# Optimization experiments

Measured on AMD Instinct MI355X. Metric: run time of the kernel, lower is better.

Reference implementation:

```python
import jax, jax.numpy as jnp
import numpy as np

NUM_CLASSES = 3
EPS = 1e-6
POS_IOU = 0.5   # assumed thresholds of utils.match_anchors_to_targets
NEG_IOU = 0.4
NEG_RATIO = 3


def _make_anchors(H, W, stride):
    sizes = np.array([3.0, 4.0, 5.0]) * stride  # 3 anchors per location
    ys = (np.arange(H) + 0.5) * stride
    xs = (np.arange(W) + 0.5) * stride
    cy, cx = np.meshgrid(ys, xs, indexing='ij')
    cx = cx[:, :, None]
    cy = cy[:, :, None]
    s = sizes[None, None, :]
    boxes = np.stack([cx - s / 2, cy - s / 2, cx + s / 2, cy + s / 2], axis=-1)  # [H,W,A,4]
    return boxes.reshape(-1, 4).astype(np.float32)


def setup_inputs() -> dict:
    key = jax.random.key(0)
    B, G, A, C = 64, 32, 3, NUM_CLASSES
    scales = [(128, 128, 8), (64, 64, 16), (32, 32, 32)]
    ks = jax.random.split(key, 6)
    inp = {}
    for i, (H, W, s) in enumerate(scales):
        inp[f'pred{i}'] = jax.random.normal(ks[i], (B, A * (5 + C), H, W), jnp.float32)
        inp[f'anchors{i}'] = jnp.asarray(_make_anchors(H, W, s))
    c = jax.random.uniform(ks[3], (B, G, 2), minval=100.0, maxval=900.0)
    wh = jax.random.uniform(ks[4], (B, G, 2), minval=16.0, maxval=200.0)
    inp['gt_boxes'] = jnp.concatenate([c - wh / 2, c + wh / 2], axis=-1)
    inp['gt_labels'] = jax.random.randint(ks[5], (B, G), 0, C)
    return inp


def _smooth_l1(x):
    ax = jnp.abs(x)
    return jnp.where(ax < 1.0, 0.5 * x * x, ax - 0.5)


def _bce_logits(x, t):
    return jnp.maximum(x, 0.0) - x * t + jnp.log1p(jnp.exp(-jnp.abs(x)))


def _pairwise_iou(a, b):  # a [N,4], b [G,4] -> [N,G]
    lt = jnp.maximum(a[:, None, :2], b[None, :, :2])
    rb = jnp.minimum(a[:, None, 2:], b[None, :, 2:])
    wh = jnp.clip(rb - lt, 0.0)
    inter = wh[..., 0] * wh[..., 1]
    area_a = (a[:, 2] - a[:, 0]) * (a[:, 3] - a[:, 1])
    area_b = (b[:, 2] - b[:, 0]) * (b[:, 3] - b[:, 1])
    return inter / (area_a[:, None] + area_b[None, :] - inter + 1e-9)


def _per_image(p, anc, gtb, gtl):
    # p: [N, 5+C], anc: [N,4], gtb: [G,4], gtl: [G]
    iou = _pairwise_iou(anc, gtb)
    best_iou = jnp.max(iou, axis=1)
    best_idx = jnp.argmax(iou, axis=1)
    m_boxes = gtb[best_idx]
    m_labels = gtl[best_idx]
    pos = best_iou >= POS_IOU
    neg = best_iou < NEG_IOU
    posf = pos.astype(p.dtype)

    ax = (anc[:, 0] + anc[:, 2]) * 0.5
    ay = (anc[:, 1] + anc[:, 3]) * 0.5
    aw = jnp.maximum(anc[:, 2] - anc[:, 0], EPS)
    ah = jnp.maximum(anc[:, 3] - anc[:, 1], EPS)
    gx = (m_boxes[:, 0] + m_boxes[:, 2]) * 0.5
    gy = (m_boxes[:, 1] + m_boxes[:, 3]) * 0.5
    gw = jnp.maximum(m_boxes[:, 2] - m_boxes[:, 0], EPS)
    gh = jnp.maximum(m_boxes[:, 3] - m_boxes[:, 1], EPS)
    t_tx = (gx - ax) / aw
    t_ty = (gy - ay) / ah
    t_tw = jnp.log(gw / aw)
    t_th = jnp.log(gh / ah)

    loc = (posf * (_smooth_l1(p[:, 0] - t_tx) + _smooth_l1(p[:, 1] - t_ty)
                   + _smooth_l1(p[:, 2] - t_tw) + _smooth_l1(p[:, 3] - t_th))).sum()

    obj_all = _bce_logits(p[:, 4], posf)
    # hard negative mining on detached loss: top (3*max(1,num_pos)) negatives
    num_pos = pos.sum()
    num_keep = NEG_RATIO * jnp.maximum(1, num_pos)
    neg_loss = jnp.where(neg, jax.lax.stop_gradient(obj_all), -1e9)
    order = jnp.argsort(-neg_loss)
    N = order.shape[0]
    ranks = jnp.zeros((N,), dtype=jnp.int32).at[order].set(jnp.arange(N, dtype=jnp.int32))
    selected = neg & (ranks < num_keep)
    obj = (obj_all * (posf + selected.astype(p.dtype))).sum()

    logp = jax.nn.log_softmax(p[:, 5:], axis=-1)
    tgt = jnp.maximum(m_labels, 0)
    ce = -jnp.take_along_axis(logp, tgt[:, None], axis=1)[:, 0]
    cls = (posf * ce).sum()
    return loc, obj, cls


def reference(pred0, pred1, pred2, anchors0, anchors1, anchors2, gt_boxes, gt_labels):
    B = pred0.shape[0]
    C = NUM_CLASSES
    total = jnp.float32(0.0)
    for pred, anc in ((pred0, anchors0), (pred1, anchors1), (pred2, anchors2)):
        N = anc.shape[0]
        p = pred.transpose(0, 2, 3, 1).reshape(B, N, 5 + C)  # [B, H*W*A, 5+C]
        loc, obj, cls = jax.vmap(lambda pb, gb, gl, a=anc: _per_image(pb, a, gb, gl))(
            p, gt_boxes, gt_labels)
        total = total + loc.sum() + obj.sum() + cls.sum()
    return total / jnp.maximum(1.0, float(B))
```

## Files before the change

### kernel.cpp

```cpp
#include <hip/hip_runtime.h>
#include <math.h>

#define BLK 256
#define SBLK 1024
#define NBINS 2048
#define HREP 2
#define CSH 42
#define QMASK ((1ULL << CSH) - 1ULL)

__device__ __forceinline__ float bce_logits(float x, float t){
    return fmaxf(x, 0.f) - x * t + log1pf(expf(-fabsf(x)));
}
__device__ __forceinline__ float smooth_l1(float x){
    float ax = fabsf(x);
    return ax < 1.f ? 0.5f * x * x : ax - 0.5f;
}

__global__ __launch_bounds__(BLK)
void det_map_all(const float* __restrict__ pred0,
                 const float* __restrict__ pred1,
                 const float* __restrict__ pred2,
                 const float* __restrict__ gtb,
                 const int*   __restrict__ gtl,
                 unsigned long long* __restrict__ hist,
                 float* __restrict__ loss_slot,
                 int*   __restrict__ pcnt_slot,
                 unsigned* __restrict__ done_cnt,
                 int B)
{
    const int b  = blockIdx.y;
    const int bx = blockIdx.x;

    const float* pred; int s, qloc, P, logW; float stride_f;
    if (bx < 48){      s=0; pred=pred0; P=16384; logW=7; stride_f= 8.f; qloc= bx      << 8; }
    else if (bx < 60){ s=1; pred=pred1; P= 4096; logW=6; stride_f=16.f; qloc=(bx-48) << 8; }
    else {             s=2; pred=pred2; P= 1024; logW=5; stride_f=32.f; qloc=(bx-60) << 8; }

    const int tid = threadIdx.x;
    const int lq  = 2*logW - 2;
    const int Q4  = 1 << lq;
    const int a   = qloc >> lq;
    const int pix0 = (qloc - a*Q4 + tid) << 2;

    const float half = 0.5f * (float)(3 + a) * stride_f;

    const int pixLo = (qloc - a*Q4) << 2;
    const int y0 = pixLo >> logW, y1 = (pixLo + BLK*4 - 1) >> logW;
    const float ymin = ((float)y0 + 0.5f) * stride_f - half;
    const float ymax = ((float)y1 + 0.5f) * stride_f + half;

    __shared__ float4 sg[32];
    __shared__ float  sarea[32];
    __shared__ int    sl[32];
    __shared__ int    s_cnt;
    __shared__ unsigned long long sh_h[HREP][NBINS];

    for (int i = tid; i < HREP * NBINS; i += BLK)
        ((unsigned long long*)sh_h)[i] = 0ULL;

    {
        bool keep = false; float4 G;
        if (tid < 32){
            G = ((const float4*)gtb)[b * 32 + tid];
            keep = (G.y < ymax) && (G.w > ymin);
        }
        unsigned long long m = __ballot(keep);
        if (tid < 64){
            if (keep){
                int idx = (int)__popcll(m & ((1ULL << tid) - 1ULL));
                sg[idx] = G;
                sarea[idx] = (G.z - G.x) * (G.w - G.y);
                sl[idx] = gtl[b * 32 + tid];
            }
            if (tid == 0) s_cnt = (int)__popcll(m);
        }
    }
    __syncthreads();
    const int cnt = s_cnt;

    const int x0 = pix0 & ((1 << logW) - 1);
    const int y  = pix0 >> logW;
    const float cy = ((float)y + 0.5f) * stride_f;
    const float Ay = cy - half, Ay2 = cy + half;
    const float area_a = (2.f * half) * (2.f * half);

    float ax[4], az[4];
    #pragma unroll
    for (int j = 0; j < 4; ++j){
        float cx = ((float)(x0 + j) + 0.5f) * stride_f;
        ax[j] = cx - half; az[j] = cx + half;
    }

    float bi[4] = {-1.f, -1.f, -1.f, -1.f};
    float bd[4] = { 1.f,  1.f,  1.f,  1.f};
    int   bg[4] = {0, 0, 0, 0};

    for (int g = 0; g < cnt; ++g){
        const float4 G = sg[g];
        const float sab = area_a + sarea[g];
        const float h = fmaxf(fminf(Ay2, G.w) - fmaxf(Ay, G.y), 0.f);
        #pragma unroll
        for (int j = 0; j < 4; ++j){
            float wdt = fmaxf(fminf(az[j], G.z) - fmaxf(ax[j], G.x), 0.f);
            float inter = wdt * h;
            float d = (sab - inter) + 1e-9f;
            if (inter * bd[j] > bi[j] * d){ bi[j] = inter; bd[j] = d; bg[j] = g; }
        }
    }

    const size_t cP = (size_t)P;
    const float* pp = pred + ((size_t)b * 24 + (size_t)a * 8) * cP + (size_t)pix0;
    const float4 p4v = *(const float4*)(pp + 4 * cP);
    const float p4a[4] = {p4v.x, p4v.y, p4v.z, p4v.w};

    const int rep = tid & (HREP - 1);
    float loss = 0.f; int pc = 0;
    #pragma unroll
    for (int j = 0; j < 4; ++j){
        const bool pos = 2.f * bi[j] >= bd[j];
        const bool neg = bi[j] < 0.4f * bd[j];
        if (neg){
            float v = bce_logits(p4a[j], 0.f);
            int bin = min((int)(v * 512.f), NBINS - 1);
            unsigned long long pq = (1ULL << CSH) |
                (unsigned long long)(unsigned)(int)(v * 4194304.f);
            atomicAdd(&sh_h[rep][bin], pq);
        }
        if (pos){
            pc++;
            const float4 G = sg[bg[j]];
            float axc = (ax[j] + az[j]) * 0.5f, ayc = (Ay + Ay2) * 0.5f;
            float aw = fmaxf(az[j] - ax[j], 1e-6f), ah = fmaxf(Ay2 - Ay, 1e-6f);
            float gxc = (G.x + G.z) * 0.5f, gyc = (G.y + G.w) * 0.5f;
            float gw = fmaxf(G.z - G.x, 1e-6f), gh = fmaxf(G.w - G.y, 1e-6f);
            float p0 = pp[0 * cP + j];
            float p1 = pp[1 * cP + j];
            float p2 = pp[2 * cP + j];
            float p3 = pp[3 * cP + j];
            loss += smooth_l1(p0 - (gxc - axc) / aw);
            loss += smooth_l1(p1 - (gyc - ayc) / ah);
            loss += smooth_l1(p2 - logf(gw / aw));
            loss += smooth_l1(p3 - logf(gh / ah));
            loss += bce_logits(p4a[j], 1.f);
            float c0 = pp[5 * cP + j];
            float c1 = pp[6 * cP + j];
            float c2 = pp[7 * cP + j];
            float m = fmaxf(c0, fmaxf(c1, c2));
            float lse = m + logf(expf(c0 - m) + expf(c1 - m) + expf(c2 - m));
            int tg = sl[bg[j]];
            float ct = (tg == 0) ? c0 : ((tg == 1) ? c1 : c2);
            loss += lse - ct;
        }
    }

    for (int off = 32; off > 0; off >>= 1){
        loss += __shfl_down(loss, off);
        pc   += __shfl_down(pc, off);
    }
    __shared__ float wsum[BLK / 64];
    __shared__ int   wcnt[BLK / 64];
    if ((tid & 63) == 0){ wsum[tid >> 6] = loss; wcnt[tid >> 6] = pc; }
    __syncthreads();

    unsigned long long* gh = hist + (size_t)(s * B + b) * NBINS;
    for (int i = tid; i < NBINS; i += BLK){
        unsigned long long t = sh_h[0][i] + sh_h[1][i];
        if (t) atomicAdd(&gh[i], t);
    }

    if (tid == 0){
        float S = 0.f; int C = 0;
        for (int i = 0; i < BLK / 64; ++i){ S += wsum[i]; C += wcnt[i]; }
        loss_slot[b * 63 + bx] = S;
        pcnt_slot[b * 63 + bx] = C;
        if (b == 0 && bx == 0) *done_cnt = 0u;
    }
}

__global__ __launch_bounds__(SBLK)
void det_select(const unsigned long long* __restrict__ hist,
                const float* __restrict__ loss_slot,
                const int* __restrict__ pcnt_slot,
                double* __restrict__ slice_tot,
                unsigned* __restrict__ done_cnt,
                float* __restrict__ out, int B)
{
    const int sb = blockIdx.x;
    const int s = sb / B, b = sb - s * B;

    const int tid = threadIdx.x;
    const int lane = tid & 63, w = tid >> 6;

    __shared__ unsigned long long waveT[16];
    __shared__ unsigned long long waveOff[17];
    __shared__ double sh_sel;
    __shared__ float sh_ml;
    __shared__ int sh_done, sh_K, sh_last;

    {
        const int nb   = (s == 0) ? 48 : (s == 1) ? 12 : 3;
        const int off0 = b * 63 + ((s == 0) ? 0 : (s == 1) ? 48 : 60);
        float ml = 0.f; int C = 0;
        if (tid < nb){ ml = loss_slot[off0 + tid]; C = pcnt_slot[off0 + tid]; }
        if (tid < 64){
            for (int off = 32; off > 0; off >>= 1){
                ml += __shfl_down(ml, off);
                C  += __shfl_down(C, off);
            }
            if (tid == 0){ sh_ml = ml; sh_K = 3 * max(1, C); sh_done = 0; }
        }
    }

    const int bhi = NBINS - 1 - 2 * tid;
    const unsigned long long c0p = hist[(size_t)sb * NBINS + bhi];
    const unsigned long long c1p = hist[(size_t)sb * NBINS + bhi - 1];
    const unsigned long long pair = c0p + c1p;
    unsigned long long ci = pair;
    #pragma unroll
    for (int off = 1; off < 64; off <<= 1){
        unsigned long long cu = __shfl_up(ci, off);
        if (lane >= off) ci += cu;
    }
    if (lane == 63) waveT[w] = ci;
    __syncthreads();
    if (tid == 0){
        unsigned long long acc = 0ULL;
        #pragma unroll
        for (int i = 0; i < 16; ++i){ waveOff[i] = acc; acc += waveT[i]; }
        waveOff[16] = acc;
        if (sh_K >= (int)(acc >> CSH)){
            sh_done = 1;
            sh_sel = (double)(acc & QMASK) * (1.0 / 4194304.0);
        }
    }
    __syncthreads();

    if (!sh_done){
        const int K = sh_K;
        const unsigned long long giP = waveOff[w] + ci;
        const unsigned long long geP = giP - pair;
        const int gi = (int)(giP >> CSH);
        const int ge = (int)(geP >> CSH);
        if (ge < K && K <= gi){
            const int c0 = (int)(c0p >> CSH);
            int bin, aboveC; unsigned long long aboveQ;
            if (ge + c0 >= K){ bin = bhi;     aboveC = ge;      aboveQ = geP & QMASK; }
            else             { bin = bhi - 1; aboveC = ge + c0; aboveQ = (geP + c0p) & QMASK; }
            float thresh = (float)bin * (1.f / 512.f);
            sh_sel = (double)aboveQ * (1.0 / 4194304.0)
                   + (double)(K - aboveC) * (double)thresh;
        }
        __syncthreads();
    }

    if (tid == 0){
        slice_tot[sb] = (double)sh_ml + sh_sel;
        __threadfence();
        unsigned t = atomicAdd(done_cnt, 1u);
        sh_last = (t == (unsigned)(gridDim.x - 1));
        if (sh_last) __threadfence();
    }
    __syncthreads();
    if (sh_last){
        double p = (tid < 3 * B) ? slice_tot[tid] : 0.0;
        for (int off = 32; off > 0; off >>= 1) p += __shfl_down(p, off);
        __shared__ double wred[16];
        if (lane == 0) wred[w] = p;
        __syncthreads();
        if (tid == 0){
            double tot = 0.0;
            for (int i = 0; i < 16; ++i) tot += wred[i];
            out[0] = (float)(tot / (double)B);
        }
    }
}

extern "C" void kernel_launch(void* const* d_in, const int* in_sizes, int n_in,
                              void* d_out, int out_size, void* d_ws, size_t ws_size,
                              hipStream_t stream)
{
    const float* gtb = (const float*)d_in[6];
    const int*   gtl = (const int*)d_in[7];
    const int B = in_sizes[6] / (32 * 4);

    unsigned* done      = (unsigned*)d_ws;
    double*   slice_tot = (double*)((char*)d_ws + 64);
    float*    loss_slot = (float*)((char*)d_ws + 2048);
    int*      pcnt_slot = (int*)((char*)d_ws + 2048 + 16384);
    unsigned long long* hist = (unsigned long long*)((char*)d_ws + 36864);

    hipMemsetAsync(hist, 0, (size_t)(3 * B) * NBINS * sizeof(unsigned long long), stream);
    det_map_all<<<dim3(63, B), BLK, 0, stream>>>(
        (const float*)d_in[0], (const float*)d_in[2], (const float*)d_in[4],
        gtb, gtl, hist, loss_slot, pcnt_slot, done, B);
    det_select<<<dim3(3 * B), SBLK, 0, stream>>>(
        hist, loss_slot, pcnt_slot, slice_tot, done, (float*)d_out, B);
}
```

Before: 204.2 us.

## Fuse histogram select into map kernel via per-slice last-block ticket

Removes the separate det_select launch. The last block to finish each (scale, image) slice, identified by an atomic per-slice ticket, now does the top-K negative selection from the global histogram, and a global done counter picks the block that reduces the final total. The scan now runs with 256 threads over 8 bins each instead of 1024 threads over 2 bins. One memset clears both the counters and the histograms. This saves a kernel launch and its gap, at the cost of extra fences and a serial tail in the last block of each slice.

```diff
diff --git a/kernel.cpp b/kernel.cpp
--- a/kernel.cpp
+++ b/kernel.cpp
@@ -2,7 +2,6 @@
 #include <math.h>
 
 #define BLK 256
-#define SBLK 1024
 #define NBINS 2048
 #define HREP 2
 #define CSH 42
@@ -17,26 +16,31 @@
 }
 
 __global__ __launch_bounds__(BLK)
-void det_map_all(const float* __restrict__ pred0,
-                 const float* __restrict__ pred1,
-                 const float* __restrict__ pred2,
-                 const float* __restrict__ gtb,
-                 const int*   __restrict__ gtl,
-                 unsigned long long* __restrict__ hist,
-                 float* __restrict__ loss_slot,
-                 int*   __restrict__ pcnt_slot,
-                 unsigned* __restrict__ done_cnt,
-                 int B)
+void det_fused(const float* __restrict__ pred0,
+               const float* __restrict__ pred1,
+               const float* __restrict__ pred2,
+               const float* __restrict__ gtb,
+               const int*   __restrict__ gtl,
+               unsigned long long* __restrict__ hist,
+               unsigned* __restrict__ slice_tick,
+               unsigned* __restrict__ done_cnt,
+               float* __restrict__ loss_slot,
+               int*   __restrict__ pcnt_slot,
+               double* __restrict__ slice_tot,
+               float* __restrict__ out, int B)
 {
     const int b  = blockIdx.y;
     const int bx = blockIdx.x;
 
-    const float* pred; int s, qloc, P, logW; float stride_f;
-    if (bx < 48){      s=0; pred=pred0; P=16384; logW=7; stride_f= 8.f; qloc= bx      << 8; }
-    else if (bx < 60){ s=1; pred=pred1; P= 4096; logW=6; stride_f=16.f; qloc=(bx-48) << 8; }
-    else {             s=2; pred=pred2; P= 1024; logW=5; stride_f=32.f; qloc=(bx-60) << 8; }
-
-    const int tid = threadIdx.x;
+    const float* pred; int s, qloc, P, logW, nb, sbase; float stride_f;
+    if (bx < 48){      s=0; pred=pred0; P=16384; logW=7; stride_f= 8.f; qloc= bx      << 8; nb=48; sbase=0;  }
+    else if (bx < 60){ s=1; pred=pred1; P= 4096; logW=6; stride_f=16.f; qloc=(bx-48) << 8; nb=12; sbase=48; }
+    else {             s=2; pred=pred2; P= 1024; logW=5; stride_f=32.f; qloc=(bx-60) << 8; nb=3;  sbase=60; }
+
+    const int tid  = threadIdx.x;
+    const int lane = tid & 63, w = tid >> 6;
+    const int sb   = s * B + b;
+
     const int lq  = 2*logW - 2;
     const int Q4  = 1 << lq;
     const int a   = qloc >> lq;
@@ -54,6 +58,14 @@
     __shared__ int    sl[32];
     __shared__ int    s_cnt;
     __shared__ unsigned long long sh_h[HREP][NBINS];
+    __shared__ float wsum[BLK / 64];
+    __shared__ int   wcnt[BLK / 64];
+    __shared__ int   sh_fin, sh_done, sh_K, sh_last;
+    __shared__ float sh_ml;
+    __shared__ double sh_sel;
+    __shared__ unsigned long long waveT[BLK / 64];
+    __shared__ unsigned long long waveOff[BLK / 64];
+    __shared__ double wred[BLK / 64];
 
     for (int i = tid; i < HREP * NBINS; i += BLK)
         ((unsigned long long*)sh_h)[i] = 0ULL;
@@ -157,15 +169,13 @@
         loss += __shfl_down(loss, off);
         pc   += __shfl_down(pc, off);
     }
-    __shared__ float wsum[BLK / 64];
-    __shared__ int   wcnt[BLK / 64];
     if ((tid & 63) == 0){ wsum[tid >> 6] = loss; wcnt[tid >> 6] = pc; }
     __syncthreads();
 
-    unsigned long long* gh = hist + (size_t)(s * B + b) * NBINS;
+    unsigned long long* ghm = hist + (size_t)sb * NBINS;
     for (int i = tid; i < NBINS; i += BLK){
         unsigned long long t = sh_h[0][i] + sh_h[1][i];
-        if (t) atomicAdd(&gh[i], t);
+        if (t) atomicAdd(&ghm[i], t);
     }
 
     if (tid == 0){
@@ -173,33 +183,21 @@
         for (int i = 0; i < BLK / 64; ++i){ S += wsum[i]; C += wcnt[i]; }
         loss_slot[b * 63 + bx] = S;
         pcnt_slot[b * 63 + bx] = C;
-        if (b == 0 && bx == 0) *done_cnt = 0u;
-    }
-}
-
-__global__ __launch_bounds__(SBLK)
-void det_select(const unsigned long long* __restrict__ hist,
-                const float* __restrict__ loss_slot,
-                const int* __restrict__ pcnt_slot,
-                double* __restrict__ slice_tot,
-                unsigned* __restrict__ done_cnt,
-                float* __restrict__ out, int B)
-{
-    const int sb = blockIdx.x;
-    const int s = sb / B, b = sb - s * B;
-
-    const int tid = threadIdx.x;
-    const int lane = tid & 63, w = tid >> 6;
-
-    __shared__ unsigned long long waveT[16];
-    __shared__ unsigned long long waveOff[17];
-    __shared__ double sh_sel;
-    __shared__ float sh_ml;
-    __shared__ int sh_done, sh_K, sh_last;
+    }
+
+    __syncthreads();
+    if (tid == 0){
+        __threadfence();
+        unsigned t = atomicAdd(&slice_tick[sb], 1u);
+        sh_fin = (t == (unsigned)(nb - 1));
+    }
+    __syncthreads();
+    if (!sh_fin) return;
+
+    __threadfence();
 
     {
-        const int nb   = (s == 0) ? 48 : (s == 1) ? 12 : 3;
-        const int off0 = b * 63 + ((s == 0) ? 0 : (s == 1) ? 48 : 60);
+        const int off0 = b * 63 + sbase;
         float ml = 0.f; int C = 0;
         if (tid < nb){ ml = loss_slot[off0 + tid]; C = pcnt_slot[off0 + tid]; }
         if (tid < 64){
@@ -207,15 +205,16 @@
                 ml += __shfl_down(ml, off);
                 C  += __shfl_down(C, off);
             }
-            if (tid == 0){ sh_ml = ml; sh_K = 3 * max(1, C); sh_done = 0; }
-        }
-    }
-
-    const int bhi = NBINS - 1 - 2 * tid;
-    const unsigned long long c0p = hist[(size_t)sb * NBINS + bhi];
-    const unsigned long long c1p = hist[(size_t)sb * NBINS + bhi - 1];
-    const unsigned long long pair = c0p + c1p;
-    unsigned long long ci = pair;
+            if (tid == 0){ sh_ml = ml; sh_K = 3 * max(1, C); }
+        }
+    }
+
+    const int btop = NBINS - 1 - 8 * tid;
+    unsigned long long c[8];
+    unsigned long long L = 0ULL;
+    #pragma unroll
+    for (int k = 0; k < 8; ++k){ c[k] = ghm[btop - k]; L += c[k]; }
+    unsigned long long ci = L;
     #pragma unroll
     for (int off = 1; off < 64; off <<= 1){
         unsigned long long cu = __shfl_up(ci, off);
@@ -226,29 +225,30 @@
     if (tid == 0){
         unsigned long long acc = 0ULL;
         #pragma unroll
-        for (int i = 0; i < 16; ++i){ waveOff[i] = acc; acc += waveT[i]; }
-        waveOff[16] = acc;
+        for (int i = 0; i < BLK / 64; ++i){ waveOff[i] = acc; acc += waveT[i]; }
         if (sh_K >= (int)(acc >> CSH)){
             sh_done = 1;
             sh_sel = (double)(acc & QMASK) * (1.0 / 4194304.0);
+        } else {
+            sh_done = 0;
         }
     }
     __syncthreads();
 
     if (!sh_done){
         const int K = sh_K;
-        const unsigned long long giP = waveOff[w] + ci;
-        const unsigned long long geP = giP - pair;
-        const int gi = (int)(giP >> CSH);
-        const int ge = (int)(geP >> CSH);
-        if (ge < K && K <= gi){
-            const int c0 = (int)(c0p >> CSH);
-            int bin, aboveC; unsigned long long aboveQ;
-            if (ge + c0 >= K){ bin = bhi;     aboveC = ge;      aboveQ = geP & QMASK; }
-            else             { bin = bhi - 1; aboveC = ge + c0; aboveQ = (geP + c0p) & QMASK; }
-            float thresh = (float)bin * (1.f / 512.f);
-            sh_sel = (double)aboveQ * (1.0 / 4194304.0)
-                   + (double)(K - aboveC) * (double)thresh;
+        unsigned long long run = waveOff[w] + ci - L;
+        #pragma unroll
+        for (int k = 0; k < 8; ++k){
+            const unsigned long long cc = c[k];
+            const int rc  = (int)(run >> CSH);
+            const int rc2 = (int)((run + cc) >> CSH);
+            if (rc < K && K <= rc2){
+                float thresh = (float)(btop - k) * (1.f / 512.f);
+                sh_sel = (double)(run & QMASK) * (1.0 / 4194304.0)
+                       + (double)(K - rc) * (double)thresh;
+            }
+            run += cc;
         }
         __syncthreads();
     }
@@ -257,19 +257,18 @@
         slice_tot[sb] = (double)sh_ml + sh_sel;
         __threadfence();
         unsigned t = atomicAdd(done_cnt, 1u);
-        sh_last = (t == (unsigned)(gridDim.x - 1));
-        if (sh_last) __threadfence();
+        sh_last = (t == (unsigned)(3 * B - 1));
     }
     __syncthreads();
     if (sh_last){
+        __threadfence();
         double p = (tid < 3 * B) ? slice_tot[tid] : 0.0;
         for (int off = 32; off > 0; off >>= 1) p += __shfl_down(p, off);
-        __shared__ double wred[16];
         if (lane == 0) wred[w] = p;
         __syncthreads();
         if (tid == 0){
             double tot = 0.0;
-            for (int i = 0; i < 16; ++i) tot += wred[i];
+            for (int i = 0; i < BLK / 64; ++i) tot += wred[i];
             out[0] = (float)(tot / (double)B);
         }
     }
@@ -283,16 +282,19 @@
     const int*   gtl = (const int*)d_in[7];
     const int B = in_sizes[6] / (32 * 4);
 
-    unsigned* done      = (unsigned*)d_ws;
-    double*   slice_tot = (double*)((char*)d_ws + 64);
-    float*    loss_slot = (float*)((char*)d_ws + 2048);
-    int*      pcnt_slot = (int*)((char*)d_ws + 2048 + 16384);
-    unsigned long long* hist = (unsigned long long*)((char*)d_ws + 36864);
-
-    hipMemsetAsync(hist, 0, (size_t)(3 * B) * NBINS * sizeof(unsigned long long), stream);
-    det_map_all<<<dim3(63, B), BLK, 0, stream>>>(
+    unsigned* done       = (unsigned*)d_ws;
+    unsigned* slice_tick = (unsigned*)((char*)d_ws + 64);
+    unsigned long long* hist = (unsigned long long*)((char*)d_ws + 4096);
+    const size_t hist_bytes = (size_t)(3 * B) * NBINS * sizeof(unsigned long long);
+
+    char* after = (char*)d_ws + 4096 + hist_bytes;
+    double* slice_tot = (double*)after;
+    float*  loss_slot = (float*)(after + 2048);
+    int*    pcnt_slot = (int*)(after + 2048 + 16384);
+
+    hipMemsetAsync(d_ws, 0, 4096 + hist_bytes, stream);
+    det_fused<<<dim3(63, B), BLK, 0, stream>>>(
         (const float*)d_in[0], (const float*)d_in[2], (const float*)d_in[4],
-        gtb, gtl, hist, loss_slot, pcnt_slot, done, B);
-    det_select<<<dim3(3 * B), SBLK, 0, stream>>>(
-        hist, loss_slot, pcnt_slot, slice_tot, done, (float*)d_out, B);
+        gtb, gtl, hist, slice_tick, done,
+        loss_slot, pcnt_slot, slice_tot, (float*)d_out, B);
 }
```

New measurement: 372.6 us. 82.5% more time.
